# Optimization experiments

Measured on AMD Instinct MI355X. Metric: run time of the kernel, lower is better.

The kernel has to match this reference:

```python
import jax, jax.numpy as jnp
import numpy as np

# ---- configuration matching init_kwargs ----
D_IN, D_HID, D_OUT = 4096, 4096, 4096
INTRINSIC = 1024            # size of trainable vector V
BATCH = 512
Q = float(min(np.log(60000.0) ** 2 / INTRINSIC, 1.0))  # fastJL_vars: q = min(ln(60000)^2/d, 1)

PARAM_SHAPES = {
    'W1': (D_HID, D_IN),   # nn.Linear weight is (out, in)
    'b1': (D_HID,),
    'W2': (D_OUT, D_HID),
    'b2': (D_OUT,),
}

def _next_pow2(n):
    return 1 << int(np.ceil(np.log2(n)))

def fwht(x):
    """Fast Walsh-Hadamard transform over a length-2^k vector.
    Mirrors fast_walsh_hadamard_torched: at step i, split axis i of the
    [2]*k view into halves a,b and concatenate (a+b, a-b)."""
    n = x.shape[0]
    steps = int(round(np.log2(n)))
    for i in range(steps):
        y = x.reshape(2 ** i, 2, -1)
        a, b = y[:, 0], y[:, 1]
        x = jnp.stack([a + b, a - b], axis=1).reshape(n)
    return x

def fastjl(V, D, PP, shape):
    """ret = (1/dd) * (PP * FWHT(D * pad(V, LL)))[:DD], reshaped to param shape."""
    LL = D.shape[0]
    dd = V.shape[0]
    DD = int(np.prod(shape))
    v_pad = jnp.zeros((LL,), V.dtype).at[:dd].set(V)
    h = fwht(D * v_pad)
    return ((PP * h)[:DD] / dd).reshape(shape)

def setup_inputs() -> dict:
    key = jax.random.key(0)
    ks = jax.random.split(key, 4 + 3 * len(PARAM_SHAPES) + len(PARAM_SHAPES))
    inp = {}
    inp['x'] = jax.random.normal(ks[0], (BATCH, D_IN), dtype=jnp.float32)
    inp['V'] = jax.random.normal(ks[1], (INTRINSIC,), dtype=jnp.float32) * 0.01
    i = 2
    for name, shape in PARAM_SHAPES.items():
        # initial (frozen) parameter values
        scale = 1.0 / np.sqrt(shape[-1]) if len(shape) > 1 else 0.0
        inp[name + '_init'] = jax.random.normal(ks[i], shape, dtype=jnp.float32) * scale
        LL = _next_pow2(int(np.prod(shape)))
        # D: Rademacher +-1
        rad = jax.random.bernoulli(ks[i + 1], 0.5, (LL,))
        inp['D_' + name] = jnp.where(rad, 1.0, -1.0).astype(jnp.float32)
        # PP = B * R, B ~ Bernoulli(1-q), R ~ N(0, (1/q)^2)
        B = jax.random.bernoulli(ks[i + 2], 1.0 - Q, (LL,)).astype(jnp.float32)
        R = jax.random.normal(ks[i + 3], (LL,), dtype=jnp.float32) * (1.0 / Q)
        inp['PP_' + name] = B * R
        i += 4
    return inp

def reference(x, V, W1_init, b1_init, W2_init, b2_init,
              D_W1, PP_W1, D_b1, PP_b1, D_W2, PP_W2, D_b2, PP_b2):
    # Reconstruct each wrapped-module parameter: init + FastJL(V)
    W1 = W1_init + fastjl(V, D_W1, PP_W1, PARAM_SHAPES['W1'])
    b1 = b1_init + fastjl(V, D_b1, PP_b1, PARAM_SHAPES['b1'])
    W2 = W2_init + fastjl(V, D_W2, PP_W2, PARAM_SHAPES['W2'])
    b2 = b2_init + fastjl(V, D_b2, PP_b2, PARAM_SHAPES['b2'])
    # wrapped module forward: Linear -> ReLU -> Linear
    h = jax.nn.relu(x @ W1.T + b1)
    return h @ W2.T + b2
```

## Files before the change

kernel.cpp:

```cpp
#include <hip/hip_runtime.h>
#include <hip/hip_bf16.h>
#include <stdint.h>

typedef unsigned short u16;
typedef __attribute__((ext_vector_type(8))) short short8;
typedef __attribute__((ext_vector_type(4))) float f32x4;

__device__ __forceinline__ uint32_t f2bf(float f) {
    union { float f; uint32_t u; } c; c.f = f;
    uint32_t u = c.u;
    u += 0x7fffu + ((u >> 16) & 1u);
    return u >> 16;
}

__device__ __forceinline__ void glds16(const void* g, void* l) {
    __builtin_amdgcn_global_load_lds(
        (const __attribute__((address_space(1))) uint32_t*)g,
        (__attribute__((address_space(3))) uint32_t*)l,
        16, 0, 0);
}

__device__ __forceinline__ uint2 wrow2(float4 wi, float4 pp, float4 gv) {
    uint32_t lo = f2bf(wi.x + pp.x * gv.x) | (f2bf(wi.y + pp.y * gv.y) << 16);
    uint32_t hi = f2bf(wi.z + pp.z * gv.z) | (f2bf(wi.w + pp.w * gv.w) << 16);
    return make_uint2(lo, hi);
}

__global__ void fwht_g_kernel(const float* __restrict__ V,
                              const float* __restrict__ D0, const float* __restrict__ D1,
                              const float* __restrict__ D2, const float* __restrict__ D3,
                              float* __restrict__ g) {
    __shared__ float s[1024];
    int t = threadIdx.x;
    const float* D = (blockIdx.x == 0) ? D0 : (blockIdx.x == 1) ? D1 :
                     (blockIdx.x == 2) ? D2 : D3;
    s[t] = D[t] * V[t];
    __syncthreads();
    #pragma unroll
    for (int st = 512; st >= 1; st >>= 1) {
        float a = s[t];
        float b = s[t ^ st];
        __syncthreads();
        s[t] = (t & st) ? (b - a) : (a + b);
        __syncthreads();
    }
    g[blockIdx.x * 1024 + t] = s[t] * (1.0f / 1024.0f);
}

__global__ void bias_kernel(const float* __restrict__ init, const float* __restrict__ PP,
                            const float* __restrict__ g, float* __restrict__ out, int n) {
    int i = blockIdx.x * blockDim.x + threadIdx.x;
    if (i < n) out[i] = init[i] + PP[i] * g[i & 1023];
}

__global__ void cast_kernel(const float* __restrict__ in, u16* __restrict__ out, int n4) {
    int i = blockIdx.x * blockDim.x + threadIdx.x;
    if (i >= n4) return;
    float4 v = ((const float4*)in)[i];
    uint32_t lo = f2bf(v.x) | (f2bf(v.y) << 16);
    uint32_t hi = f2bf(v.z) | (f2bf(v.w) << 16);
    ((uint2*)out)[i] = make_uint2(lo, hi);
}

__global__ __launch_bounds__(256, 2) void gemm_fused(const u16* __restrict__ A,
                                                     const float* __restrict__ Winit,
                                                     const float* __restrict__ PP,
                                                     const float* __restrict__ gvec,
                                                     float* __restrict__ P,
                                                     int M, int N, int K, int Kslice) {
    constexpr int BM = 256, BN = 64, BK = 64;
    __shared__ u16 As[2][BM * BK];
    __shared__ u16 Bs[2][BN * BK];

    const int t    = threadIdx.x;
    const int wid  = t >> 6;
    const int lane = t & 63;
    const int fr   = lane & 15;
    const int fq   = lane >> 4;

    const int bn = blockIdx.x, bm = blockIdx.y, sk = blockIdx.z;
    const int k_beg = sk * Kslice;
    const int npair = (Kslice / BK) / 2;

    const u16* Abase = A + (size_t)(bm * BM) * K;

    const int rB = t >> 4;
    const int cB = (t & 15) * 4;
    const float* Wb = Winit + (size_t)(bn * BN + rB) * K;
    const float* Pb = PP    + (size_t)(bn * BN + rB) * K;
    const size_t rstride = (size_t)16 * K;

    float4 w00, w01, w02, w03, p00, p01, p02, p03;
    float4 w10, w11, w12, w13, p10, p11, p12, p13;

#define PF_W0(k0) do {                                        \
        const float* wp_ = Wb + (k0) + cB;                    \
        const float* qp_ = Pb + (k0) + cB;                    \
        w00 = *(const float4*)(wp_);                          \
        w01 = *(const float4*)(wp_ + rstride);                \
        w02 = *(const float4*)(wp_ + 2 * rstride);            \
        w03 = *(const float4*)(wp_ + 3 * rstride);            \
        p00 = *(const float4*)(qp_);                          \
        p01 = *(const float4*)(qp_ + rstride);                \
        p02 = *(const float4*)(qp_ + 2 * rstride);            \
        p03 = *(const float4*)(qp_ + 3 * rstride);            \
    } while (0)

#define PF_W1(k0) do {                                        \
        const float* wp_ = Wb + (k0) + cB;                    \
        const float* qp_ = Pb + (k0) + cB;                    \
        w10 = *(const float4*)(wp_);                          \
        w11 = *(const float4*)(wp_ + rstride);                \
        w12 = *(const float4*)(wp_ + 2 * rstride);            \
        w13 = *(const float4*)(wp_ + 3 * rstride);            \
        p10 = *(const float4*)(qp_);                          \
        p11 = *(const float4*)(qp_ + rstride);                \
        p12 = *(const float4*)(qp_ + 2 * rstride);            \
        p13 = *(const float4*)(qp_ + 3 * rstride);            \
    } while (0)

#define WRITE_B0(k0, buf) do {                                                    \
        float4 gv_ = *(const float4*)(gvec + (((k0) + cB) & 1023));               \
        *(uint2*)(Bs[buf] + (rB +  0) * BK + cB) = wrow2(w00, p00, gv_);          \
        *(uint2*)(Bs[buf] + (rB + 16) * BK + cB) = wrow2(w01, p01, gv_);          \
        *(uint2*)(Bs[buf] + (rB + 32) * BK + cB) = wrow2(w02, p02, gv_);          \
        *(uint2*)(Bs[buf] + (rB + 48) * BK + cB) = wrow2(w03, p03, gv_);          \
    } while (0)

#define WRITE_B1(k0, buf) do {                                                    \
        float4 gv_ = *(const float4*)(gvec + (((k0) + cB) & 1023));               \
        *(uint2*)(Bs[buf] + (rB +  0) * BK + cB) = wrow2(w10, p10, gv_);          \
        *(uint2*)(Bs[buf] + (rB + 16) * BK + cB) = wrow2(w11, p11, gv_);          \
        *(uint2*)(Bs[buf] + (rB + 32) * BK + cB) = wrow2(w12, p12, gv_);          \
        *(uint2*)(Bs[buf] + (rB + 48) * BK + cB) = wrow2(w13, p13, gv_);          \
    } while (0)

#define STAGE_A(k0, buf) do {                                                     \
        _Pragma("unroll")                                                         \
        for (int q_ = 0; q_ < 8; ++q_) {                                          \
            int L_ = q_ * 256 + t;                                                \
            int row_ = L_ >> 3;                                                   \
            int cg_ = (L_ & 7) * 8;                                               \
            glds16(Abase + (size_t)row_ * K + (k0) + cg_, As[buf] + L_ * 8);      \
        }                                                                         \
    } while (0)

#define MFMA_STEP(buf) do {                                                       \
        __builtin_amdgcn_s_setprio(1);                                            \
        _Pragma("unroll")                                                         \
        for (int ks_ = 0; ks_ < 2; ++ks_) {                                       \
            short8 a_[4], b_[4];                                                  \
            _Pragma("unroll")                                                     \
            for (int m_ = 0; m_ < 4; ++m_)                                        \
                a_[m_] = *(const short8*)(As[buf] +                               \
                          (wid * 64 + m_ * 16 + fr) * BK + ks_ * 32 + fq * 8);    \
            _Pragma("unroll")                                                     \
            for (int n_ = 0; n_ < 4; ++n_)                                        \
                b_[n_] = *(const short8*)(Bs[buf] +                               \
                          (n_ * 16 + fr) * BK + ks_ * 32 + fq * 8);               \
            _Pragma("unroll")                                                     \
            for (int m_ = 0; m_ < 4; ++m_)                                        \
                _Pragma("unroll")                                                 \
                for (int n_ = 0; n_ < 4; ++n_)                                    \
                    acc[m_][n_] = __builtin_amdgcn_mfma_f32_16x16x32_bf16(        \
                        a_[m_], b_[n_], acc[m_][n_], 0, 0, 0);                    \
        }                                                                         \
        __builtin_amdgcn_s_setprio(0);                                            \
    } while (0)

    f32x4 acc[4][4];
    #pragma unroll
    for (int m = 0; m < 4; ++m)
        #pragma unroll
        for (int n = 0; n < 4; ++n)
            acc[m][n] = (f32x4){0.f, 0.f, 0.f, 0.f};

    PF_W0(k_beg);
    PF_W1(k_beg + BK);
    STAGE_A(k_beg, 0);
    WRITE_B0(k_beg, 0);
    __syncthreads();

    int kk = k_beg;
    #pragma unroll 1
    for (int p = 0; p < npair - 1; ++p, kk += 2 * BK) {
        PF_W0(kk + 2 * BK);
        STAGE_A(kk + BK, 1);
        WRITE_B1(kk + BK, 1);
        MFMA_STEP(0);
        __syncthreads();
        PF_W1(kk + 3 * BK);
        STAGE_A(kk + 2 * BK, 0);
        WRITE_B0(kk + 2 * BK, 0);
        MFMA_STEP(1);
        __syncthreads();
    }
    STAGE_A(kk + BK, 1);
    WRITE_B1(kk + BK, 1);
    MFMA_STEP(0);
    __syncthreads();
    MFMA_STEP(1);

#undef PF_W0
#undef PF_W1
#undef WRITE_B0
#undef WRITE_B1
#undef STAGE_A
#undef MFMA_STEP

    float* Pp = P + (size_t)sk * M * N;
    #pragma unroll
    for (int m = 0; m < 4; ++m) {
        int grow0 = bm * BM + wid * 64 + m * 16 + fq * 4;
        #pragma unroll
        for (int n = 0; n < 4; ++n) {
            int gcol = bn * BN + n * 16 + fr;
            #pragma unroll
            for (int j = 0; j < 4; ++j)
                Pp[(size_t)(grow0 + j) * N + gcol] = acc[m][n][j];
        }
    }
}

template <typename OutT, bool RELU, int S>
__global__ void reduce_kernel(const float* __restrict__ P, const float* __restrict__ bias,
                              OutT* __restrict__ out, int MN, int N) {
    int i = blockIdx.x * blockDim.x + threadIdx.x;
    if (i * 4 >= MN) return;
    int e = i * 4;
    int col = e & (N - 1);
    float4 acc = ((const float4*)(P + e))[0];
    #pragma unroll
    for (int s = 1; s < S; ++s) {
        float4 p = ((const float4*)(P + (size_t)s * MN + e))[0];
        acc.x += p.x; acc.y += p.y; acc.z += p.z; acc.w += p.w;
    }
    float4 bv = *((const float4*)(bias + col));
    acc.x += bv.x; acc.y += bv.y; acc.z += bv.z; acc.w += bv.w;
    if (RELU) {
        acc.x = fmaxf(acc.x, 0.f); acc.y = fmaxf(acc.y, 0.f);
        acc.z = fmaxf(acc.z, 0.f); acc.w = fmaxf(acc.w, 0.f);
    }
    if constexpr (sizeof(OutT) == 2) {
        uint32_t lo = f2bf(acc.x) | (f2bf(acc.y) << 16);
        uint32_t hi = f2bf(acc.z) | (f2bf(acc.w) << 16);
        ((uint2*)out)[i] = make_uint2(lo, hi);
    } else {
        ((float4*)out)[i] = acc;
    }
}

extern "C" void kernel_launch(void* const* d_in, const int* in_sizes, int n_in,
                              void* d_out, int out_size, void* d_ws, size_t ws_size,
                              hipStream_t stream) {
    (void)in_sizes; (void)n_in; (void)out_size; (void)ws_size;

    const float* x       = (const float*)d_in[0];
    const float* V       = (const float*)d_in[1];
    const float* W1_init = (const float*)d_in[2];
    const float* D_W1    = (const float*)d_in[3];
    const float* PP_W1   = (const float*)d_in[4];
    const float* b1_init = (const float*)d_in[5];
    const float* D_b1    = (const float*)d_in[6];
    const float* PP_b1   = (const float*)d_in[7];
    const float* W2_init = (const float*)d_in[8];
    const float* D_W2    = (const float*)d_in[9];
    const float* PP_W2   = (const float*)d_in[10];
    const float* b2_init = (const float*)d_in[11];
    const float* D_b2    = (const float*)d_in[12];
    const float* PP_b2   = (const float*)d_in[13];

    constexpr size_t MB = 1024 * 1024;
    char* ws = (char*)d_ws;
    float* g    = (float*)(ws);
    float* b1w  = (float*)(ws + 16384);
    float* b2w  = (float*)(ws + 32768);
    u16*   xb   = (u16*)(ws + 65536);
    u16*   hb   = (u16*)(ws + 65536 + 4 * MB);
    float* Pbuf = (float*)(ws + 65536 + 8 * MB);

    const int M = 512, N = 4096, K = 4096, S = 4, Kslice = K / S;

    fwht_g_kernel<<<4, 1024, 0, stream>>>(V, D_W1, D_b1, D_W2, D_b2, g);
    bias_kernel<<<4, 1024, 0, stream>>>(b1_init, PP_b1, g + 1024, b1w, 4096);
    bias_kernel<<<4, 1024, 0, stream>>>(b2_init, PP_b2, g + 3072, b2w, 4096);
    cast_kernel<<<2048, 256, 0, stream>>>(x, xb, M * K / 4);

    gemm_fused<<<dim3(N / 64, M / 256, S), 256, 0, stream>>>(xb, W1_init, PP_W1, g, Pbuf, M, N, K, Kslice);
    reduce_kernel<u16, true, S><<<M * N / 4 / 256, 256, 0, stream>>>(Pbuf, b1w, hb, M * N, N);

    gemm_fused<<<dim3(N / 64, M / 256, S), 256, 0, stream>>>(hb, W2_init, PP_W2, g + 2048, Pbuf, M, N, K, Kslice);
    reduce_kernel<float, false, S><<<M * N / 4 / 256, 256, 0, stream>>>(Pbuf, b2w, (float*)d_out, M * N, N);
}
```

Baseline: 144.2 us.

## Swizzle LDS tiles and restructure GEMM pipeline with partial vmcnt waits

Applies an XOR swizzle to the A and B shared-memory tiles so that MFMA fragment reads avoid LDS bank conflicts. It also reorders the main loop so A staging and the W/PP prefetch are issued before the MFMAs and the B tile is converted after them. Full __syncthreads is replaced by a barrier that waits only on older vector loads (vmcnt(8)), keeping prefetches in flight. The loop tail is folded into the main loop by clamping prefetch offsets, which adds redundant loads on the final iteration and relies on a hand-tuned vmcnt value being correct.

```diff
diff --git a/kernel.cpp b/kernel.cpp
--- a/kernel.cpp
+++ b/kernel.cpp
@@ -77,15 +77,19 @@
     const int lane = t & 63;
     const int fr   = lane & 15;
     const int fq   = lane >> 4;
+    const int rx   = (fr & 7) << 4;
 
     const int bn = blockIdx.x, bm = blockIdx.y, sk = blockIdx.z;
     const int k_beg = sk * Kslice;
+    const int kmax  = k_beg + Kslice - BK;
     const int npair = (Kslice / BK) / 2;
 
     const u16* Abase = A + (size_t)(bm * BM) * K;
 
-    const int rB = t >> 4;
-    const int cB = (t & 15) * 4;
+    const int rB  = t >> 4;
+    const int cB  = (t & 15) * 4;
+    const int cb8 = (t & 15) * 8;
+    const int wxor = (rB & 7) << 4;
     const float* Wb = Winit + (size_t)(bn * BN + rB) * K;
     const float* Pb = PP    + (size_t)(bn * BN + rB) * K;
     const size_t rstride = (size_t)16 * K;
@@ -121,43 +125,47 @@
 
 #define WRITE_B0(k0, buf) do {                                                    \
         float4 gv_ = *(const float4*)(gvec + (((k0) + cB) & 1023));               \
-        *(uint2*)(Bs[buf] + (rB +  0) * BK + cB) = wrow2(w00, p00, gv_);          \
-        *(uint2*)(Bs[buf] + (rB + 16) * BK + cB) = wrow2(w01, p01, gv_);          \
-        *(uint2*)(Bs[buf] + (rB + 32) * BK + cB) = wrow2(w02, p02, gv_);          \
-        *(uint2*)(Bs[buf] + (rB + 48) * BK + cB) = wrow2(w03, p03, gv_);          \
+        char* Bp_ = (char*)Bs[buf];                                               \
+        *(uint2*)(Bp_ + ((((rB +  0) * 128 + cb8)) ^ wxor)) = wrow2(w00, p00, gv_); \
+        *(uint2*)(Bp_ + ((((rB + 16) * 128 + cb8)) ^ wxor)) = wrow2(w01, p01, gv_); \
+        *(uint2*)(Bp_ + ((((rB + 32) * 128 + cb8)) ^ wxor)) = wrow2(w02, p02, gv_); \
+        *(uint2*)(Bp_ + ((((rB + 48) * 128 + cb8)) ^ wxor)) = wrow2(w03, p03, gv_); \
     } while (0)
 
 #define WRITE_B1(k0, buf) do {                                                    \
         float4 gv_ = *(const float4*)(gvec + (((k0) + cB) & 1023));               \
-        *(uint2*)(Bs[buf] + (rB +  0) * BK + cB) = wrow2(w10, p10, gv_);          \
-        *(uint2*)(Bs[buf] + (rB + 16) * BK + cB) = wrow2(w11, p11, gv_);          \
-        *(uint2*)(Bs[buf] + (rB + 32) * BK + cB) = wrow2(w12, p12, gv_);          \
-        *(uint2*)(Bs[buf] + (rB + 48) * BK + cB) = wrow2(w13, p13, gv_);          \
+        char* Bp_ = (char*)Bs[buf];                                               \
+        *(uint2*)(Bp_ + ((((rB +  0) * 128 + cb8)) ^ wxor)) = wrow2(w10, p10, gv_); \
+        *(uint2*)(Bp_ + ((((rB + 16) * 128 + cb8)) ^ wxor)) = wrow2(w11, p11, gv_); \
+        *(uint2*)(Bp_ + ((((rB + 32) * 128 + cb8)) ^ wxor)) = wrow2(w12, p12, gv_); \
+        *(uint2*)(Bp_ + ((((rB + 48) * 128 + cb8)) ^ wxor)) = wrow2(w13, p13, gv_); \
     } while (0)
 
 #define STAGE_A(k0, buf) do {                                                     \
         _Pragma("unroll")                                                         \
         for (int q_ = 0; q_ < 8; ++q_) {                                          \
-            int L_ = q_ * 256 + t;                                                \
+            int L_ = q_ * 256 + t;                           \
             int row_ = L_ >> 3;                                                   \
-            int cg_ = (L_ & 7) * 8;                                               \
-            glds16(Abase + (size_t)row_ * K + (k0) + cg_, As[buf] + L_ * 8);      \
+            int cg_ = (L_ & 7) ^ (row_ & 7);              \
+            glds16(Abase + (size_t)row_ * K + (k0) + cg_ * 8, As[buf] + L_ * 8);  \
         }                                                                         \
     } while (0)
 
 #define MFMA_STEP(buf) do {                                                       \
+        const char* Ap_ = (const char*)As[buf];                                   \
+        const char* Bp_ = (const char*)Bs[buf];                                   \
         __builtin_amdgcn_s_setprio(1);                                            \
         _Pragma("unroll")                                                         \
         for (int ks_ = 0; ks_ < 2; ++ks_) {                                       \
+            const int co_ = (ks_ * 64 + fq * 16) ^ rx;                            \
             short8 a_[4], b_[4];                                                  \
             _Pragma("unroll")                                                     \
             for (int m_ = 0; m_ < 4; ++m_)                                        \
-                a_[m_] = *(const short8*)(As[buf] +                               \
-                          (wid * 64 + m_ * 16 + fr) * BK + ks_ * 32 + fq * 8);    \
+                a_[m_] = *(const short8*)(Ap_ +                                   \
+                          (wid * 64 + m_ * 16 + fr) * 128 + co_);                 \
             _Pragma("unroll")                                                     \
             for (int n_ = 0; n_ < 4; ++n_)                                        \
-                b_[n_] = *(const short8*)(Bs[buf] +                               \
-                          (n_ * 16 + fr) * BK + ks_ * 32 + fq * 8);               \
+                b_[n_] = *(const short8*)(Bp_ + (n_ * 16 + fr) * 128 + co_);      \
             _Pragma("unroll")                                                     \
             for (int m_ = 0; m_ < 4; ++m_)                                        \
                 _Pragma("unroll")                                                 \
@@ -168,6 +176,12 @@
         __builtin_amdgcn_s_setprio(0);                                            \
     } while (0)
 
+#define WAIT_BAR() do {                                                           \
+        asm volatile("s_waitcnt vmcnt(8) lgkmcnt(0)" ::: "memory");               \
+        __builtin_amdgcn_s_barrier();                                             \
+        __builtin_amdgcn_sched_barrier(0);                                        \
+    } while (0)
+
     f32x4 acc[4][4];
     #pragma unroll
     for (int m = 0; m < 4; ++m)
@@ -176,30 +190,37 @@
             acc[m][n] = (f32x4){0.f, 0.f, 0.f, 0.f};
 
     PF_W0(k_beg);
+    __builtin_amdgcn_sched_barrier(0);
+    STAGE_A(k_beg, 0);
+    __builtin_amdgcn_sched_barrier(0);
     PF_W1(k_beg + BK);
-    STAGE_A(k_beg, 0);
+    __builtin_amdgcn_sched_barrier(0);
     WRITE_B0(k_beg, 0);
-    __syncthreads();
+    WAIT_BAR();
 
     int kk = k_beg;
     #pragma unroll 1
-    for (int p = 0; p < npair - 1; ++p, kk += 2 * BK) {
-        PF_W0(kk + 2 * BK);
-        STAGE_A(kk + BK, 1);
-        WRITE_B1(kk + BK, 1);
+    for (int p = 0; p < npair; ++p, kk += 2 * BK) {
+        const int nk = kk + BK;
+        int n2 = kk + 2 * BK; if (n2 > kmax) n2 = kmax;
+        int n3 = kk + 3 * BK; if (n3 > kmax) n3 = kmax;
+
+        STAGE_A(nk, 1);
+        __builtin_amdgcn_sched_barrier(0);
+        PF_W0(n2);
+        __builtin_amdgcn_sched_barrier(0);
         MFMA_STEP(0);
-        __syncthreads();
-        PF_W1(kk + 3 * BK);
-        STAGE_A(kk + 2 * BK, 0);
-        WRITE_B0(kk + 2 * BK, 0);
+        WRITE_B1(nk, 1);
+        WAIT_BAR();
+
+        STAGE_A(n2, 0);
+        __builtin_amdgcn_sched_barrier(0);
+        PF_W1(n3);
+        __builtin_amdgcn_sched_barrier(0);
         MFMA_STEP(1);
-        __syncthreads();
-    }
-    STAGE_A(kk + BK, 1);
-    WRITE_B1(kk + BK, 1);
-    MFMA_STEP(0);
-    __syncthreads();
-    MFMA_STEP(1);
+        WRITE_B0(n2, 0);
+        WAIT_BAR();
+    }
 
 #undef PF_W0
 #undef PF_W1
@@ -207,6 +228,7 @@
 #undef WRITE_B1
 #undef STAGE_A
 #undef MFMA_STEP
+#undef WAIT_BAR
 
     float* Pp = P + (size_t)sk * M * N;
     #pragma unroll
```

After: 130.1 us. -9.7%, faster.
